# Performance work log

Hardware: AMD Instinct MI355X
Metric: run time of the kernel (lower is better)

## Reference

```python
import jax, jax.numpy as jnp
import numpy as np

B, L, D, H, N = 8, 2048, 128, 4, 2
DK = D // H          # 32
DFF = 2 * D          # 256 (dff = d * 2 in source)


def _init_proj(key, shape):
    # matches torch init: uniform in [-s, s], s = sqrt(6/(fan_in+fan_out)) of last two dims
    s = np.sqrt(6.0 / (shape[-1] + shape[-2]))
    return jax.random.uniform(key, shape, jnp.float32, -s, s)


def setup_inputs() -> dict:
    key = jax.random.key(0)
    ks = jax.random.split(key, 8)
    x = jax.random.normal(ks[0], (B, L, D), jnp.float32)
    mask = jnp.ones((B, L), jnp.float32)
    Wq = _init_proj(ks[1], (N, H, D, DK))
    Wk = _init_proj(ks[2], (N, H, D, DK))
    Wv = _init_proj(ks[3], (N, H, D, DK))
    Wo = _init_proj(ks[4], (N, H * DK, D))
    W1 = _init_proj(ks[5], (N, D, DFF))
    b1 = jnp.zeros((N, 1, 1, DFF), jnp.float32)
    W2 = _init_proj(ks[6], (N, DFF, D))
    b2 = jnp.zeros((N, 1, 1, D), jnp.float32)
    return {"x": x, "mask": mask, "Wq": Wq, "Wk": Wk, "Wv": Wv,
            "Wo": Wo, "W1": W1, "b1": b1, "W2": W2, "b2": b2}


def reference(x, mask, Wq, Wk, Wv, Wo, W1, b1, W2, b2):
    # Eval-mode forward (no attention dropout-mask trick, no FFN dropout).
    neg = jnp.finfo(x.dtype).min
    m2 = mask[:, :, None] * mask[:, None, :]              # [B, L, L]
    add_mask = (1.0 - m2)[:, None, :, :] * neg            # [B, 1, L, L]
    bsz, max_len, _ = x.shape
    for i in range(N):  # small fixed layer loop
        q = jnp.einsum('bld,hde->bhle', x, Wq[i])         # [B,H,L,DK]
        k = jnp.einsum('bld,hde->bhle', x, Wk[i])
        v = jnp.einsum('bld,hde->bhle', x, Wv[i])
        A = jnp.einsum('bhqe,bhke->bhqk', q, k) + add_mask  # note: no 1/sqrt(dk), as in source
        A = jax.nn.softmax(A, axis=-1)                    # [B,H,L,L]
        o = jnp.einsum('bhqk,bhke->bqhe', A, v)           # [B,L,H,DK]
        o = o.reshape(bsz, max_len, H * DK) @ Wo[i]       # [B,L,D]
        x = (o + x) / 2
        f = jax.nn.gelu(x @ W1[i] + b1[i], approximate=False)  # torch F.gelu is exact erf
        f = f @ W2[i] + b2[i]
        x = (f + x) / 2
    return x
```

## Files before the change

### kernel.cpp

```cpp
#include <hip/hip_runtime.h>
#include <math.h>

#define BB 8
#define LL 2048
#define DD 128
#define HH 4
#define DKK 32
#define DFFF 256

#define NEGMIN (-3.402823466e38f)
#define LOG2E 1.44269504088896f

typedef _Float16 f16;
typedef _Float16 f16x4 __attribute__((ext_vector_type(4)));
typedef _Float16 f16x8 __attribute__((ext_vector_type(8)));
typedef __fp16 h16x2 __attribute__((ext_vector_type(2)));
typedef float f32x4 __attribute__((ext_vector_type(4)));

union PKU { h16x2 h2[2]; f16x4 v; };

__global__ __launch_bounds__(256) void xcvt_kernel(const float* __restrict__ x,
                                                   f16* __restrict__ xh) {
  const int i = (blockIdx.x * 256 + threadIdx.x) * 8;
  float4 v0 = *(const float4*)(x + i);
  float4 v1 = *(const float4*)(x + i + 4);
  f16x8 h;
  h[0] = (f16)v0.x; h[1] = (f16)v0.y; h[2] = (f16)v0.z; h[3] = (f16)v0.w;
  h[4] = (f16)v1.x; h[5] = (f16)v1.y; h[6] = (f16)v1.z; h[7] = (f16)v1.w;
  *(f16x8*)(xh + i) = h;
}

__global__ __launch_bounds__(256) void maskchk_kernel(
    const float* __restrict__ mask, int* __restrict__ flags) {
  __shared__ int wok[4];
  const int b = blockIdx.x, t = threadIdx.x;
  bool ok = true;
  for (int i = t; i < LL; i += 256) ok &= (mask[b * LL + i] == 1.f);
  const bool all_ok = __all(ok);
  if ((t & 63) == 0) wok[t >> 6] = all_ok ? 1 : 0;
  __syncthreads();
  if (t == 0) flags[b] = wok[0] & wok[1] & wok[2] & wok[3];
}

__global__ __launch_bounds__(256) void wconv_kernel(
    const float* __restrict__ Wq, const float* __restrict__ Wk,
    const float* __restrict__ Wv, const float* __restrict__ Wo,
    const float* __restrict__ W1, const float* __restrict__ W2,
    f16* __restrict__ wt) {
  const int idx = blockIdx.x * 256 + threadIdx.x;
  const int i = idx >> 17;
  const int r = idx & 131071;
  float val;
  if (r < 49152) {
    const int sel = r / 16384;
    const int rr = r & 16383;
    const int n = rr >> 7, k = rr & 127;
    const float* W = (sel == 0) ? Wq : (sel == 1) ? Wk : Wv;
    val = W[((size_t)(i * 4 + (n >> 5)) * 128 + k) * 32 + (n & 31)];
  } else if (r < 65536) {
    const int r2 = r - 49152;
    const int n = r2 >> 7, k = r2 & 127;
    val = Wo[i * 16384 + k * 128 + n];
  } else if (r < 98304) {
    const int r2 = r - 65536;
    const int n = r2 >> 7, k = r2 & 127;
    val = W1[i * 32768 + k * 256 + n];
  } else {
    const int r2 = r - 98304;
    const int n = r2 >> 8, k = r2 & 255;
    val = W2[i * 32768 + k * 128 + n];
  }
  wt[idx] = (f16)val;
}

__global__ __launch_bounds__(256) void qkv_kernel(
    const f16* __restrict__ xh, const f16* __restrict__ wqkvT,
    f16* __restrict__ qh, f16* __restrict__ kh, f16* __restrict__ vth) {
  const int t = threadIdx.x;
  const int wave = t >> 6, lane = t & 63;
  const int g = lane >> 4, c = lane & 15;
  const int r0g = blockIdx.x * 64 + wave * 16;
  const int b4 = (r0g >> 11) * 4;
  const int l0 = r0g & 2047;

  f16x8 a[4];
#pragma unroll
  for (int kt = 0; kt < 4; ++kt)
    a[kt] = *(const f16x8*)(xh + (size_t)(r0g + c) * 128 + kt * 32 + g * 8);

#pragma unroll
  for (int sel = 0; sel < 2; ++sel) {
    const f16* wT = wqkvT + sel * 16384;
    f16* out = (sel == 0) ? qh : kh;
#pragma unroll
    for (int nt = 0; nt < 8; ++nt) {
      f32x4 acc = {0.f, 0.f, 0.f, 0.f};
#pragma unroll
      for (int kt = 0; kt < 4; ++kt) {
        f16x8 bfrag = *(const f16x8*)(wT + (nt * 16 + c) * 128 + kt * 32 + g * 8);
        acc = __builtin_amdgcn_mfma_f32_16x16x32_f16(a[kt], bfrag, acc, 0, 0, 0);
      }
      const int h = nt >> 1, e = (nt & 1) * 16 + c;
#pragma unroll
      for (int r = 0; r < 4; ++r)
        out[((size_t)(b4 + h) * LL + l0 + 4 * g + r) * DKK + e] = (f16)acc[r];
    }
  }
  {
    const f16* wT = wqkvT + 2 * 16384;
#pragma unroll
    for (int nt = 0; nt < 8; ++nt) {
      f32x4 acc = {0.f, 0.f, 0.f, 0.f};
#pragma unroll
      for (int kt = 0; kt < 4; ++kt) {
        f16x8 afrag = *(const f16x8*)(wT + (nt * 16 + c) * 128 + kt * 32 + g * 8);
        acc = __builtin_amdgcn_mfma_f32_16x16x32_f16(afrag, a[kt], acc, 0, 0, 0);
      }
#pragma unroll
      for (int r = 0; r < 4; ++r) {
        const int eg = nt * 16 + 4 * g + r;
        vth[((size_t)(b4 + (eg >> 5)) * DKK + (eg & 31)) * LL + l0 + c] =
            (f16)acc[r];
      }
    }
  }
}

__global__ __launch_bounds__(256, 4) void attn_kernel(
    const f16* __restrict__ qh, const f16* __restrict__ kh,
    const f16* __restrict__ vth, const float* __restrict__ mask,
    const int* __restrict__ bflags, f16* __restrict__ o) {
  __shared__ f16 Vt[4][2][32][72];
  const int t = threadIdx.x;
  const int wave = t >> 6, lane = t & 63;
  const int g = lane >> 4, c = lane & 15;

  const int flat = blockIdx.x;
  const int xcd = flat & 7, slot = flat >> 3;
  const int bh = xcd * 4 + (slot >> 4);
  const int qb = slot & 15;
  const int b = bh >> 2;
  const int qw = qb * 128 + wave * 32;
  const bool nomask_b = (bflags[b] != 0);

  f16x8 qfrag[2];
  float mqv[2] = {1.f, 1.f};
#pragma unroll
  for (int qt = 0; qt < 2; ++qt)
    qfrag[qt] =
        *(const f16x8*)(qh + ((size_t)bh * LL + qw + qt * 16 + c) * DKK + g * 8);
  if (!nomask_b) {
#pragma unroll
    for (int qt = 0; qt < 2; ++qt) mqv[qt] = mask[b * LL + qw + qt * 16 + c];
  }

  f32x4 o4[2][2];
  float m[2], l[2];
#pragma unroll
  for (int qt = 0; qt < 2; ++qt) {
    m[qt] = -3.0e38f; l[qt] = 0.f;
#pragma unroll
    for (int dt = 0; dt < 2; ++dt)
#pragma unroll
      for (int r = 0; r < 4; ++r) o4[qt][dt][r] = 0.f;
  }

  const f16* kp = kh + (size_t)bh * LL * DKK + (size_t)c * DKK + g * 8;
  const int vd = lane >> 3, vseg = lane & 7;
  const f16* vp = vth + (size_t)bh * DKK * LL + (size_t)vd * LL + vseg * 8;

#define LOADK(DST, KT)                                       \
  {                                                          \
    const f16* _p = kp + (size_t)(KT) * 64 * DKK;            \
    DST[0] = *(const f16x8*)(_p);                            \
    DST[1] = *(const f16x8*)(_p + 16 * DKK);                 \
    DST[2] = *(const f16x8*)(_p + 32 * DKK);                 \
    DST[3] = *(const f16x8*)(_p + 48 * DKK);                 \
  }
#define LOADVREG(DST, KT)                                    \
  {                                                          \
    const f16* _p = vp + (KT) * 64;                          \
    DST[0] = *(const f16x8*)(_p);                            \
    DST[1] = *(const f16x8*)(_p + 8 * LL);                   \
    DST[2] = *(const f16x8*)(_p + 16 * LL);                  \
    DST[3] = *(const f16x8*)(_p + 24 * LL);                  \
  }
#define COMMITV(SRC, BUF)                                    \
  {                                                          \
    *(f16x8*)&Vt[wave][BUF][vd][vseg * 8] = SRC[0];          \
    *(f16x8*)&Vt[wave][BUF][vd + 8][vseg * 8] = SRC[1];      \
    *(f16x8*)&Vt[wave][BUF][vd + 16][vseg * 8] = SRC[2];     \
    *(f16x8*)&Vt[wave][BUF][vd + 24][vseg * 8] = SRC[3];     \
  }

  f16x8 kbA[4], kbB[4], vr[4];

  LOADVREG(vr, 0);
  LOADK(kbA, 0);
  COMMITV(vr, 0);

  for (int kt = 0; kt < 32; ++kt) {
    const int cur = kt & 1;
    if (kt < 31) {
      LOADK(kbB, kt + 1);
      LOADVREG(vr, kt + 1);
    }
    const f16x8* kb = (kt & 1) ? kbB : kbA;

    f32x4 st[2][4];
    __builtin_amdgcn_s_setprio(1);
#pragma unroll
    for (int qt = 0; qt < 2; ++qt)
#pragma unroll
      for (int nt = 0; nt < 4; ++nt) {
        f32x4 z = {0.f, 0.f, 0.f, 0.f};
        st[qt][nt] =
            __builtin_amdgcn_mfma_f32_16x16x32_f16(kbA[nt], qfrag[qt], z, 0, 0, 0);
      }
    __builtin_amdgcn_s_setprio(0);
    (void)kb;

    if (!nomask_b) {
      const int k0 = kt * 64;
#pragma unroll
      for (int qt = 0; qt < 2; ++qt) {
        const float mq = mqv[qt];
#pragma unroll
        for (int nt = 0; nt < 4; ++nt) {
          float4 mk4 = *(const float4*)(mask + b * LL + k0 + nt * 16 + 4 * g);
          st[qt][nt][0] += (1.f - mq * mk4.x) * NEGMIN;
          st[qt][nt][1] += (1.f - mq * mk4.y) * NEGMIN;
          st[qt][nt][2] += (1.f - mq * mk4.z) * NEGMIN;
          st[qt][nt][3] += (1.f - mq * mk4.w) * NEGMIN;
        }
      }
    }

    f16x4 va[2][4];
#pragma unroll
    for (int dt = 0; dt < 2; ++dt)
#pragma unroll
      for (int nt = 0; nt < 4; ++nt)
        va[dt][nt] = *(const f16x4*)&Vt[wave][cur][dt * 16 + c][nt * 16 + 4 * g];

#pragma unroll
    for (int qt = 0; qt < 2; ++qt) {
      float vmax = fmaxf(fmaxf(st[qt][0][0], st[qt][0][1]),
                         fmaxf(st[qt][0][2], st[qt][0][3]));
#pragma unroll
      for (int nt = 1; nt < 4; ++nt)
        vmax = fmaxf(vmax, fmaxf(fmaxf(st[qt][nt][0], st[qt][nt][1]),
                                 fmaxf(st[qt][nt][2], st[qt][nt][3])));
      vmax = fmaxf(vmax, __shfl_xor(vmax, 16));
      vmax = fmaxf(vmax, __shfl_xor(vmax, 32));

      if (!__all(vmax - m[qt] <= 8.f)) {
        const float mn = fmaxf(m[qt], vmax);
        const float sc = __builtin_exp2f((m[qt] - mn) * LOG2E);
        l[qt] *= sc;
#pragma unroll
        for (int dt = 0; dt < 2; ++dt)
#pragma unroll
          for (int r = 0; r < 4; ++r) o4[qt][dt][r] *= sc;
        m[qt] = mn;
      }
      const float mn2 = m[qt] * LOG2E;

      float p[4][4];
      float psum = 0.f;
#pragma unroll
      for (int nt = 0; nt < 4; ++nt) {
#pragma unroll
        for (int r = 0; r < 4; ++r) {
          p[nt][r] = __builtin_exp2f(fmaf(st[qt][nt][r], LOG2E, -mn2));
          psum += p[nt][r];
        }
      }
      l[qt] += psum;

      __builtin_amdgcn_s_setprio(1);
#pragma unroll
      for (int nt = 0; nt < 4; ++nt) {
        PKU pk;
        pk.h2[0] = __builtin_amdgcn_cvt_pkrtz(p[nt][0], p[nt][1]);
        pk.h2[1] = __builtin_amdgcn_cvt_pkrtz(p[nt][2], p[nt][3]);
        o4[qt][0] = __builtin_amdgcn_mfma_f32_16x16x16f16(va[0][nt], pk.v,
                                                          o4[qt][0], 0, 0, 0);
        o4[qt][1] = __builtin_amdgcn_mfma_f32_16x16x16f16(va[1][nt], pk.v,
                                                          o4[qt][1], 0, 0, 0);
      }
      __builtin_amdgcn_s_setprio(0);
    }

    if (kt < 31) {
      COMMITV(vr, 1 - cur);
#pragma unroll
      for (int i = 0; i < 4; ++i) kbA[i] = kbB[i];
    }
  }
#undef LOADK
#undef LOADVREG
#undef COMMITV

  const int h = bh & 3;
#pragma unroll
  for (int qt = 0; qt < 2; ++qt) {
    float lt = l[qt];
    lt += __shfl_xor(lt, 16);
    lt += __shfl_xor(lt, 32);
    const float rdiv = 1.f / lt;
    f16* orow = o + ((size_t)b * LL + qw + qt * 16 + c) * DD + h * DKK;
#pragma unroll
    for (int dt = 0; dt < 2; ++dt) {
      f16x4 res;
      res[0] = (f16)(o4[qt][dt][0] * rdiv);
      res[1] = (f16)(o4[qt][dt][1] * rdiv);
      res[2] = (f16)(o4[qt][dt][2] * rdiv);
      res[3] = (f16)(o4[qt][dt][3] * rdiv);
      *(f16x4*)(orow + dt * 16 + g * 4) = res;
    }
  }
}

__global__ __launch_bounds__(256) void mlp_kernel(
    const f16* __restrict__ o, const float* __restrict__ x,
    const f16* __restrict__ WoT, const f16* __restrict__ W1T,
    const f16* __restrict__ W2T, const float* __restrict__ b1,
    const float* __restrict__ b2, float* __restrict__ xout,
    const f16* __restrict__ wqkvT_next,
    f16* __restrict__ qh, f16* __restrict__ kh, f16* __restrict__ vth) {
  __shared__ f16 Xm[64][136];
  __shared__ f16 Fs[64][264];
  const int t = threadIdx.x;
  const int wave = t >> 6, lane = t & 63;
  const int g = lane >> 4, c = lane & 15;
  const int mrow = wave * 16;
  const long r0 = (long)blockIdx.x * 64;

  f16x8 a1[4];
#pragma unroll
  for (int kt = 0; kt < 4; ++kt)
    a1[kt] = *(const f16x8*)(o + (r0 + mrow + c) * 128 + kt * 32 + g * 8);

  f32x4 xmreg[8];
#pragma unroll
  for (int nt = 0; nt < 8; ++nt) {
    f32x4 acc = {0.f, 0.f, 0.f, 0.f};
#pragma unroll
    for (int kt = 0; kt < 4; ++kt) {
      f16x8 bfrag = *(const f16x8*)(WoT + (nt * 16 + c) * 128 + kt * 32 + g * 8);
      acc = __builtin_amdgcn_mfma_f32_16x16x32_f16(a1[kt], bfrag, acc, 0, 0, 0);
    }
#pragma unroll
    for (int r = 0; r < 4; ++r) {
      const float xv = x[(r0 + mrow + 4 * g + r) * 128 + nt * 16 + c];
      acc[r] = (acc[r] + xv) * 0.5f;
      Xm[mrow + 4 * g + r][nt * 16 + c] = (f16)acc[r];
    }
    xmreg[nt] = acc;
  }

  f16x8 a2[4];
#pragma unroll
  for (int kt = 0; kt < 4; ++kt)
    a2[kt] = *(const f16x8*)&Xm[mrow + c][kt * 32 + g * 8];
#pragma unroll
  for (int nt = 0; nt < 16; ++nt) {
    f32x4 acc = {0.f, 0.f, 0.f, 0.f};
#pragma unroll
    for (int kt = 0; kt < 4; ++kt) {
      f16x8 bfrag = *(const f16x8*)(W1T + (nt * 16 + c) * 128 + kt * 32 + g * 8);
      acc = __builtin_amdgcn_mfma_f32_16x16x32_f16(a2[kt], bfrag, acc, 0, 0, 0);
    }
    const float bj = b1[nt * 16 + c];
#pragma unroll
    for (int r = 0; r < 4; ++r) {
      const float val = acc[r] + bj;
      Fs[mrow + 4 * g + r][nt * 16 + c] =
          (f16)(0.5f * val * (1.f + erff(val * 0.70710678118654752f)));
    }
  }

  f16x8 a3[8];
#pragma unroll
  for (int kt = 0; kt < 8; ++kt)
    a3[kt] = *(const f16x8*)&Fs[mrow + c][kt * 32 + g * 8];
#pragma unroll
  for (int nt = 0; nt < 8; ++nt) {
    f32x4 acc = {0.f, 0.f, 0.f, 0.f};
#pragma unroll
    for (int kt = 0; kt < 8; ++kt) {
      f16x8 bfrag = *(const f16x8*)(W2T + (nt * 16 + c) * 256 + kt * 32 + g * 8);
      acc = __builtin_amdgcn_mfma_f32_16x16x32_f16(a3[kt], bfrag, acc, 0, 0, 0);
    }
    const float bj = b2[nt * 16 + c];
#pragma unroll
    for (int r = 0; r < 4; ++r) {
      const float val = (acc[r] + bj + xmreg[nt][r]) * 0.5f;
      xout[(r0 + mrow + 4 * g + r) * 128 + nt * 16 + c] = val;
      Xm[mrow + 4 * g + r][nt * 16 + c] = (f16)val;
    }
  }

  if (wqkvT_next) {
    const int r0g = (int)r0 + mrow;
    const int b4 = (r0g >> 11) * 4;
    const int l0 = r0g & 2047;
    f16x8 a[4];
#pragma unroll
    for (int kt = 0; kt < 4; ++kt)
      a[kt] = *(const f16x8*)&Xm[mrow + c][kt * 32 + g * 8];

#pragma unroll
    for (int sel = 0; sel < 2; ++sel) {
      const f16* wT = wqkvT_next + sel * 16384;
      f16* out = (sel == 0) ? qh : kh;
#pragma unroll
      for (int nt = 0; nt < 8; ++nt) {
        f32x4 acc = {0.f, 0.f, 0.f, 0.f};
#pragma unroll
        for (int kt = 0; kt < 4; ++kt) {
          f16x8 bfrag =
              *(const f16x8*)(wT + (nt * 16 + c) * 128 + kt * 32 + g * 8);
          acc = __builtin_amdgcn_mfma_f32_16x16x32_f16(a[kt], bfrag, acc, 0, 0, 0);
        }
        const int h = nt >> 1, e = (nt & 1) * 16 + c;
#pragma unroll
        for (int r = 0; r < 4; ++r)
          out[((size_t)(b4 + h) * LL + l0 + 4 * g + r) * DKK + e] = (f16)acc[r];
      }
    }
    {
      const f16* wT = wqkvT_next + 2 * 16384;
#pragma unroll
      for (int nt = 0; nt < 8; ++nt) {
        f32x4 acc = {0.f, 0.f, 0.f, 0.f};
#pragma unroll
        for (int kt = 0; kt < 4; ++kt) {
          f16x8 afrag =
              *(const f16x8*)(wT + (nt * 16 + c) * 128 + kt * 32 + g * 8);
          acc = __builtin_amdgcn_mfma_f32_16x16x32_f16(afrag, a[kt], acc, 0, 0, 0);
        }
#pragma unroll
        for (int r = 0; r < 4; ++r) {
          const int eg = nt * 16 + 4 * g + r;
          vth[((size_t)(b4 + (eg >> 5)) * DKK + (eg & 31)) * LL + l0 + c] =
              (f16)acc[r];
        }
      }
    }
  }
}

extern "C" void kernel_launch(void* const* d_in, const int* in_sizes, int n_in,
                              void* d_out, int out_size, void* d_ws,
                              size_t ws_size, hipStream_t stream) {
  const float* x    = (const float*)d_in[0];
  const float* mask = (const float*)d_in[1];
  const float* Wq   = (const float*)d_in[2];
  const float* Wk   = (const float*)d_in[3];
  const float* Wv   = (const float*)d_in[4];
  const float* Wo   = (const float*)d_in[5];
  const float* W1   = (const float*)d_in[6];
  const float* b1   = (const float*)d_in[7];
  const float* W2   = (const float*)d_in[8];
  const float* b2   = (const float*)d_in[9];

  const size_t SZ = (size_t)BB * LL * DD;
  char* p = (char*)d_ws;
  f16* qh   = (f16*)p;  p += SZ * sizeof(f16);
  f16* kh   = (f16*)p;  p += SZ * sizeof(f16);
  f16* vth  = (f16*)p;  p += SZ * sizeof(f16);
  f16* ob   = (f16*)p;  p += SZ * sizeof(f16);
  f16* xh0  = (f16*)p;  p += SZ * sizeof(f16);
  f16* wt   = (f16*)p;  p += (size_t)262144 * sizeof(f16);
  int* bflags = (int*)p; p += 256;
  float* xA = (float*)p;

  wconv_kernel<<<1024, 256, 0, stream>>>(Wq, Wk, Wv, Wo, W1, W2, wt);
  xcvt_kernel<<<SZ / 8 / 256, 256, 0, stream>>>(x, xh0);
  maskchk_kernel<<<BB, 256, 0, stream>>>(mask, bflags);

  for (int i = 0; i < 2; ++i) {
    const float* xin = (i == 0) ? x : xA;
    float* xout = (i == 1) ? (float*)d_out : xA;
    const f16* qkvT_i = wt + (size_t)i * 131072;
    const f16* WoT_i  = wt + (size_t)i * 131072 + 49152;
    const f16* W1T_i  = wt + (size_t)i * 131072 + 65536;
    const f16* W2T_i  = wt + (size_t)i * 131072 + 98304;
    const float* b1_i = b1 + (long)i * DFFF;
    const float* b2_i = b2 + (long)i * DD;
    const f16* qkvT_next = (i == 0) ? (wt + 131072) : nullptr;

    if (i == 0)
      qkv_kernel<<<(BB * LL) / 64, 256, 0, stream>>>(xh0, qkvT_i, qh, kh, vth);
    attn_kernel<<<512, 256, 0, stream>>>(qh, kh, vth, mask, bflags, ob);
    mlp_kernel<<<(BB * LL) / 64, 256, 0, stream>>>(ob, xin, WoT_i, W1T_i, W2T_i,
                                                   b1_i, b2_i, xout,
                                                   qkvT_next, qh, kh, vth);
  }
}
```

Baseline: 210.7 us.

## Fold log2e into Wq, MFMA row sums, lazy max shuffle, unrolled K/V double buffer

Pre-scales Wq by log2(e) so softmax exponentials become a plain exp2 of a difference with no per-element multiply. The running row sum is now built by an extra MFMA against a ones vector, replacing scalar adds and the final cross-lane shuffle reduction. The cross-lane max shuffle only runs when the lane-local max breaks a wider rescale threshold. The K/V loop is unrolled by two with explicit A/B register buffers, which removes the per-iteration register copy. In exchange it adds MFMA work per tile and relies on the wider threshold staying safe for fp16 P values.

```diff
diff --git a/kernel.cpp b/kernel.cpp
--- a/kernel.cpp
+++ b/kernel.cpp
@@ -57,6 +57,7 @@
     const int n = rr >> 7, k = rr & 127;
     const float* W = (sel == 0) ? Wq : (sel == 1) ? Wk : Wv;
     val = W[((size_t)(i * 4 + (n >> 5)) * 128 + k) * 32 + (n & 31)];
+    if (sel == 0) val *= LOG2E;
   } else if (r < 65536) {
     const int r2 = r - 49152;
     const int n = r2 >> 7, k = r2 & 127;
@@ -154,16 +155,18 @@
     for (int qt = 0; qt < 2; ++qt) mqv[qt] = mask[b * LL + qw + qt * 16 + c];
   }
 
-  f32x4 o4[2][2];
-  float m[2], l[2];
+  f32x4 o4[2][2], lacc[2];
+  float m[2];
 #pragma unroll
   for (int qt = 0; qt < 2; ++qt) {
-    m[qt] = -3.0e38f; l[qt] = 0.f;
-#pragma unroll
-    for (int dt = 0; dt < 2; ++dt)
-#pragma unroll
-      for (int r = 0; r < 4; ++r) o4[qt][dt][r] = 0.f;
-  }
+    m[qt] = -3.0e38f;
+#pragma unroll
+    for (int r = 0; r < 4; ++r) {
+      o4[qt][0][r] = 0.f; o4[qt][1][r] = 0.f; lacc[qt][r] = 0.f;
+    }
+  }
+  f16x4 ones;
+  ones[0] = (f16)1.f; ones[1] = (f16)1.f; ones[2] = (f16)1.f; ones[3] = (f16)1.f;
 
   const f16* kp = kh + (size_t)bh * LL * DKK + (size_t)c * DKK + g * 8;
   const int vd = lane >> 3, vseg = lane & 7;
@@ -193,20 +196,9 @@
     *(f16x8*)&Vt[wave][BUF][vd + 24][vseg * 8] = SRC[3];     \
   }
 
-  f16x8 kbA[4], kbB[4], vr[4];
-
-  LOADVREG(vr, 0);
-  LOADK(kbA, 0);
-  COMMITV(vr, 0);
-
-  for (int kt = 0; kt < 32; ++kt) {
-    const int cur = kt & 1;
-    if (kt < 31) {
-      LOADK(kbB, kt + 1);
-      LOADVREG(vr, kt + 1);
-    }
-    const f16x8* kb = (kt & 1) ? kbB : kbA;
-
+  f16x8 kbA[4], kbB[4], vrA[4], vrB[4];
+
+  auto TILE = [&](const f16x8 (&kb)[4], int buf, int k0) {
     f32x4 st[2][4];
     __builtin_amdgcn_s_setprio(1);
 #pragma unroll
@@ -215,13 +207,11 @@
       for (int nt = 0; nt < 4; ++nt) {
         f32x4 z = {0.f, 0.f, 0.f, 0.f};
         st[qt][nt] =
-            __builtin_amdgcn_mfma_f32_16x16x32_f16(kbA[nt], qfrag[qt], z, 0, 0, 0);
+            __builtin_amdgcn_mfma_f32_16x16x32_f16(kb[nt], qfrag[qt], z, 0, 0, 0);
       }
     __builtin_amdgcn_s_setprio(0);
-    (void)kb;
 
     if (!nomask_b) {
-      const int k0 = kt * 64;
 #pragma unroll
       for (int qt = 0; qt < 2; ++qt) {
         const float mq = mqv[qt];
@@ -241,62 +231,68 @@
     for (int dt = 0; dt < 2; ++dt)
 #pragma unroll
       for (int nt = 0; nt < 4; ++nt)
-        va[dt][nt] = *(const f16x4*)&Vt[wave][cur][dt * 16 + c][nt * 16 + 4 * g];
+        va[dt][nt] = *(const f16x4*)&Vt[wave][buf][dt * 16 + c][nt * 16 + 4 * g];
 
 #pragma unroll
     for (int qt = 0; qt < 2; ++qt) {
-      float vmax = fmaxf(fmaxf(st[qt][0][0], st[qt][0][1]),
-                         fmaxf(st[qt][0][2], st[qt][0][3]));
-#pragma unroll
-      for (int nt = 1; nt < 4; ++nt)
-        vmax = fmaxf(vmax, fmaxf(fmaxf(st[qt][nt][0], st[qt][nt][1]),
-                                 fmaxf(st[qt][nt][2], st[qt][nt][3])));
-      vmax = fmaxf(vmax, __shfl_xor(vmax, 16));
-      vmax = fmaxf(vmax, __shfl_xor(vmax, 32));
-
-      if (!__all(vmax - m[qt] <= 8.f)) {
-        const float mn = fmaxf(m[qt], vmax);
-        const float sc = __builtin_exp2f((m[qt] - mn) * LOG2E);
-        l[qt] *= sc;
-#pragma unroll
-        for (int dt = 0; dt < 2; ++dt)
-#pragma unroll
-          for (int r = 0; r < 4; ++r) o4[qt][dt][r] *= sc;
+      float m0 = fmaxf(fmaxf(st[qt][0][0], st[qt][0][1]),
+                       fmaxf(st[qt][0][2], st[qt][0][3]));
+      float m1 = fmaxf(fmaxf(st[qt][1][0], st[qt][1][1]),
+                       fmaxf(st[qt][1][2], st[qt][1][3]));
+      float m2 = fmaxf(fmaxf(st[qt][2][0], st[qt][2][1]),
+                       fmaxf(st[qt][2][2], st[qt][2][3]));
+      float m3 = fmaxf(fmaxf(st[qt][3][0], st[qt][3][1]),
+                       fmaxf(st[qt][3][2], st[qt][3][3]));
+      const float vml = fmaxf(fmaxf(m0, m1), fmaxf(m2, m3));
+
+      if (!__all(vml - m[qt] <= 11.0f)) {
+        float vm = fmaxf(vml, __shfl_xor(vml, 16));
+        vm = fmaxf(vm, __shfl_xor(vm, 32));
+        const float mn = fmaxf(m[qt], vm);
+        const float sc = __builtin_exp2f(m[qt] - mn);
+#pragma unroll
+        for (int r = 0; r < 4; ++r) {
+          o4[qt][0][r] *= sc; o4[qt][1][r] *= sc; lacc[qt][r] *= sc;
+        }
         m[qt] = mn;
       }
-      const float mn2 = m[qt] * LOG2E;
-
-      float p[4][4];
-      float psum = 0.f;
+      const float mn = m[qt];
+
+      __builtin_amdgcn_s_setprio(1);
 #pragma unroll
       for (int nt = 0; nt < 4; ++nt) {
-#pragma unroll
-        for (int r = 0; r < 4; ++r) {
-          p[nt][r] = __builtin_exp2f(fmaf(st[qt][nt][r], LOG2E, -mn2));
-          psum += p[nt][r];
-        }
-      }
-      l[qt] += psum;
-
-      __builtin_amdgcn_s_setprio(1);
-#pragma unroll
-      for (int nt = 0; nt < 4; ++nt) {
+        const float p0 = __builtin_exp2f(st[qt][nt][0] - mn);
+        const float p1 = __builtin_exp2f(st[qt][nt][1] - mn);
+        const float p2 = __builtin_exp2f(st[qt][nt][2] - mn);
+        const float p3 = __builtin_exp2f(st[qt][nt][3] - mn);
         PKU pk;
-        pk.h2[0] = __builtin_amdgcn_cvt_pkrtz(p[nt][0], p[nt][1]);
-        pk.h2[1] = __builtin_amdgcn_cvt_pkrtz(p[nt][2], p[nt][3]);
+        pk.h2[0] = __builtin_amdgcn_cvt_pkrtz(p0, p1);
+        pk.h2[1] = __builtin_amdgcn_cvt_pkrtz(p2, p3);
         o4[qt][0] = __builtin_amdgcn_mfma_f32_16x16x16f16(va[0][nt], pk.v,
                                                           o4[qt][0], 0, 0, 0);
         o4[qt][1] = __builtin_amdgcn_mfma_f32_16x16x16f16(va[1][nt], pk.v,
                                                           o4[qt][1], 0, 0, 0);
+        lacc[qt] = __builtin_amdgcn_mfma_f32_16x16x16f16(ones, pk.v,
+                                                         lacc[qt], 0, 0, 0);
       }
       __builtin_amdgcn_s_setprio(0);
     }
-
-    if (kt < 31) {
-      COMMITV(vr, 1 - cur);
-#pragma unroll
-      for (int i = 0; i < 4; ++i) kbA[i] = kbB[i];
-    }
+  };
+
+  LOADK(kbA, 0);
+  LOADVREG(vrA, 0);
+  COMMITV(vrA, 0);
+  LOADK(kbB, 1);
+  LOADVREG(vrB, 1);
+
+  for (int k2 = 0; k2 < 16; ++k2) {
+    const int t0 = 2 * k2, t1 = 2 * k2 + 1;
+    TILE(kbA, 0, t0 * 64);
+    COMMITV(vrB, 1);
+    if (t1 + 1 < 32) { LOADK(kbA, t1 + 1); LOADVREG(vrA, t1 + 1); }
+    TILE(kbB, 1, t1 * 64);
+    if (t1 + 1 < 32) { COMMITV(vrA, 0); }
+    if (t1 + 2 < 32) { LOADK(kbB, t1 + 2); LOADVREG(vrB, t1 + 2); }
   }
 #undef LOADK
 #undef LOADVREG
@@ -305,10 +301,7 @@
   const int h = bh & 3;
 #pragma unroll
   for (int qt = 0; qt < 2; ++qt) {
-    float lt = l[qt];
-    lt += __shfl_xor(lt, 16);
-    lt += __shfl_xor(lt, 32);
-    const float rdiv = 1.f / lt;
+    const float rdiv = 1.f / lacc[qt][0];
     f16* orow = o + ((size_t)b * LL + qw + qt * 16 + c) * DD + h * DKK;
 #pragma unroll
     for (int dt = 0; dt < 2; ++dt) {
```

After: 327.3 us. 55.3% more time.
